# Optimization experiments

Measured on AMD Instinct MI355X. Metric: run time of the kernel, lower is better.

Reference implementation:

```python
import jax, jax.numpy as jnp
import numpy as np

H = 150  # hidden size
I = 1    # input size


def setup_inputs() -> dict:
    key = jax.random.key(0)
    ks = jax.random.split(key, 7)
    B, T = 512, 1024
    s_ih = 1.0 / np.sqrt(H)
    x = jax.random.normal(ks[0], (B, T, I), dtype=jnp.float32)
    # PyTorch LSTM params, gate order (i, f, g, o) stacked along first dim
    W_ih = jax.random.uniform(ks[1], (4 * H, I), jnp.float32, -s_ih, s_ih)
    W_hh = jax.random.uniform(ks[2], (4 * H, H), jnp.float32, -s_ih, s_ih)
    b_ih = jax.random.uniform(ks[3], (4 * H,), jnp.float32, -s_ih, s_ih)
    b_hh = jax.random.uniform(ks[4], (4 * H,), jnp.float32, -s_ih, s_ih)
    # final Linear(150 -> 1)
    W_out = jax.random.uniform(ks[5], (1, H), jnp.float32, -s_ih, s_ih)
    b_out = jax.random.uniform(ks[6], (1,), jnp.float32, -s_ih, s_ih)
    return {"x": x, "W_ih": W_ih, "W_hh": W_hh, "b_ih": b_ih,
            "b_hh": b_hh, "W_out": W_out, "b_out": b_out}


def _lstm_scan(x, W_ih, W_hh, b_ih, b_hh):
    B, T, _ = x.shape
    # precompute input contribution for all timesteps: [T, B, 4H]
    xg = jnp.einsum('bti,gi->tbg', x, W_ih) + (b_ih + b_hh)
    h0 = jnp.zeros((B, H), x.dtype)
    c0 = jnp.zeros((B, H), x.dtype)

    def step(carry, xg_t):
        h, c = carry
        gates = xg_t + h @ W_hh.T  # [B, 4H]
        i, f, g, o = jnp.split(gates, 4, axis=-1)
        i = jax.nn.sigmoid(i)
        f = jax.nn.sigmoid(f)
        g = jnp.tanh(g)
        o = jax.nn.sigmoid(o)
        c = f * c + i * g
        h = o * jnp.tanh(c)
        return (h, c), h

    _, hs = jax.lax.scan(step, (h0, c0), xg)  # hs: [T, B, H]
    return jnp.transpose(hs, (1, 0, 2))       # [B, T, H]


def reference(x, W_ih, W_hh, b_ih, b_hh, W_out, b_out):
    h = _lstm_scan(x, W_ih, W_hh, b_ih, b_hh)          # [B, T, H]
    return jax.nn.sigmoid(h @ W_out.T + b_out)         # [B, T, 1]
```

## Files before the change

### kernel.cpp

```cpp
#include <hip/hip_runtime.h>


typedef _Float16 half8 __attribute__((ext_vector_type(8)));
typedef int int32x8 __attribute__((ext_vector_type(8)));
typedef float f32x4 __attribute__((ext_vector_type(4)));

#define LOG2E 1.44269504088896340736f
#define TWOLOG2E 2.88539008177792681472f

__device__ inline unsigned enc_fp8(float v) {
  const float a = fabsf(v);
  const unsigned s = (__float_as_uint(v) >> 24) & 0x80u;
  const unsigned bits = __float_as_uint(a) + 0x80000u;
  const unsigned code_n = (bits >> 20) - (120u << 3);
  const unsigned code_d = (unsigned)(a * 512.0f + 0.5f);
  const unsigned code = (a < 0.015625f) ? code_d : code_n;
  return s | (code & 0x7Fu);
}

__global__
__attribute__((amdgpu_flat_work_group_size(512, 512), amdgpu_waves_per_eu(2, 2)))
void lstm_kernel(
    const float* __restrict__ x,
    const float* __restrict__ W_ih,
    const float* __restrict__ W_hh,
    const float* __restrict__ b_ih,
    const float* __restrict__ b_hh,
    const float* __restrict__ W_out,
    const float* __restrict__ b_out,
    float* __restrict__ out)
{
  const int tid  = threadIdx.x;
  const int wid  = tid >> 6;
  const int lane = tid & 63;
  const int q    = lane >> 4;
  const int b    = lane & 15;
  const int br   = b & 1;
  const int bid  = blockIdx.x;

  __shared__ __align__(16) _Float16 hbuf[2][2][168];
  __shared__ __align__(64) unsigned char h8[2][2][128];
  __shared__ _Float16 xlds[2][1032];

  for (int i = tid; i < 2*2*168; i += 512)
    (&hbuf[0][0][0])[i] = (_Float16)0.0f;
  if (tid < 128) ((unsigned*)&h8[0][0][0])[tid] = 0u;
  {
    const float4* x4 = (const float4*)(x + (size_t)bid * 2 * 1024);
    const int row = tid >> 8, c4 = tid & 255;
    float4 v = x4[row*256 + c4];
    xlds[row][c4*4+0] = (_Float16)v.x;
    xlds[row][c4*4+1] = (_Float16)v.y;
    xlds[row][c4*4+2] = (_Float16)v.z;
    xlds[row][c4*4+3] = (_Float16)v.w;
  }
  __syncthreads();
  if (tid < 4) hbuf[tid>>1][tid&1][150] = (_Float16)1.0f;
  if (tid < 2) hbuf[0][tid][151] = xlds[tid][0];
  __syncthreads();

  const int NT = (wid < 6) ? 5 : 4;
  const float bo = b_out[0];

  int32x8 wf8[5];
  half8 wf16[5];
#pragma unroll
  for (int j = 0; j < 5; ++j) {
#pragma unroll
    for (int d = 0; d < 8; ++d) wf8[j][d] = 0;
    wf16[j] = (half8)(_Float16)0.0f;
    if (j < NT) {
      const int vrow = (wid + 8*j)*16 + b;
      const int cell = vrow >> 2, gate = vrow & 3;
      const float alpha = (gate == 2) ? TWOLOG2E : -LOG2E;
#pragma unroll
      for (int d = 0; d < 8; ++d) {
        unsigned dw = 0;
#pragma unroll
        for (int c = 0; c < 4; ++c) {
          const int k = q*32 + 4*d + c;
          float w = 0.0f;
          if (vrow == 600)      w = -LOG2E * W_out[k];
          else if (cell < 150)  w = alpha * W_hh[(gate*150 + cell)*150 + k];
          dw |= enc_fp8(w) << (8*c);
        }
        wf8[j][d] = (int)dw;
      }
      half8 v;
#pragma unroll
      for (int jj = 0; jj < 8; ++jj) {
        const int k = 128 + q*8 + jj;
        float w = 0.0f;
        if (vrow == 600) {
          if (k < 150)       w = -LOG2E * W_out[k];
          else if (k == 150) w = -LOG2E * bo;
        } else if (cell < 150) {
          const int orow = gate*150 + cell;
          if (k < 150)       w = alpha * W_hh[orow*150 + k];
          else if (k == 150) w = alpha * (b_ih[orow] + b_hh[orow]);
          else if (k == 151) w = alpha * W_ih[orow];
        }
        v[jj] = (_Float16)w;
      }
      wf16[j] = v;
    }
  }

  float cst = 0.f;
  const int  e     = b >> 1;
  const int  cellm = 4*(wid + 8*e) + q;
  const bool wen   = (e < NT) && (cellm < 150);
  const bool w8    = wen && (cellm < 128);
  const bool w16   = wen && (cellm >= 128);
  const int  wc8   = (cellm < 128) ? cellm : 0;
  const int  wc16  = (cellm >= 128 && cellm < 150) ? cellm : 152;
  const bool is_x  = (wid == 7) && (q == 0) && (b < 2);
  const bool is_out= (wid == 5) && (q == 2) && (b < 2);
  float* outp = out + ((size_t)bid*2 + br) * 1024;

  const unsigned char* p8r0 = &h8[0][br][q*32];
  const unsigned char* p8r1 = &h8[1][br][q*32];
  const _Float16* p16r0 = &hbuf[0][br][128 + q*8];
  const _Float16* p16r1 = &hbuf[1][br][128 + q*8];
  unsigned char* w8p0 = &h8[0][br][wc8];
  unsigned char* w8p1 = &h8[1][br][wc8];
  _Float16* w16p0 = &hbuf[0][br][wc16];
  _Float16* w16p1 = &hbuf[1][br][wc16];
  _Float16* xw0 = &hbuf[0][br][151];
  _Float16* xw1 = &hbuf[1][br][151];
  const f32x4 ZERO = {0.f, 0.f, 0.f, 0.f};

  for (int t = 0; t <= 1024; ++t) {
    _Float16 xv = (_Float16)0.0f;
    if (is_x && t < 1023) xv = xlds[b][t+1];

    const int32x8 bf8 = *(const int32x8*)((t & 1) ? p8r1 : p8r0);
    const half8  bf16 = *(const half8*)((t & 1) ? p16r1 : p16r0);

    f32x4 acc[5];
    __builtin_amdgcn_s_setprio(1);
#pragma unroll
    for (int j = 0; j < 4; ++j) {
      acc[j] = __builtin_amdgcn_mfma_scale_f32_16x16x128_f8f6f4(
                   wf8[j], bf8, ZERO, 0, 0, 0, 0x7F7F7F7F, 0, 0x7F7F7F7F);
      acc[j] = __builtin_amdgcn_mfma_f32_16x16x32_f16(wf16[j], bf16, acc[j], 0,0,0);
    }
    if (wid < 6) {
      acc[4] = __builtin_amdgcn_mfma_scale_f32_16x16x128_f8f6f4(
                   wf8[4], bf8, ZERO, 0, 0, 0, 0x7F7F7F7F, 0, 0x7F7F7F7F);
      acc[4] = __builtin_amdgcn_mfma_f32_16x16x32_f16(wf16[4], bf16, acc[4], 0,0,0);
    } else {
      acc[4] = ZERO;
    }
    __builtin_amdgcn_s_setprio(0);

    if (is_out && t >= 1)
      outp[t-1] = __builtin_amdgcn_rcpf(1.0f + __builtin_amdgcn_exp2f(acc[4][0]));
    if (t == 1024) break;

    f32x4 g;
#pragma unroll
    for (int r = 0; r < 4; ++r) {
      const float t01 = (b & 2) ? acc[1][r] : acc[0][r];
      const float t23 = (b & 2) ? acc[3][r] : acc[2][r];
      const float t03 = (b & 4) ? t23 : t01;
      g[r] = (b & 8) ? acc[4][r] : t03;
    }
    const float ei = __builtin_amdgcn_exp2f(g[0]);
    const float ef = __builtin_amdgcn_exp2f(g[1]);
    const float eg = __builtin_amdgcn_exp2f(g[2]);
    const float eo = __builtin_amdgcn_exp2f(g[3]);
    const float A   = 1.0f + ei;
    const float F   = 1.0f + ef;
    const float G1  = eg + 1.0f;
    const float Gm  = eg - 1.0f;
    const float AG  = A * G1;
    const float num = fmaf(cst, AG, Gm * F);
    const float cn  = num * __builtin_amdgcn_rcpf(F * AG);
    cst = cn;
    const float ec = __builtin_amdgcn_exp2f(TWOLOG2E * cn);
    const float hv = (ec - 1.0f) *
                     __builtin_amdgcn_rcpf((1.0f + eo) * (ec + 1.0f));
    if (w8) {
      unsigned char* w = (t & 1) ? w8p0 : w8p1;
      *w = (unsigned char)enc_fp8(hv);
    }
    if (w16) {
      _Float16* w = (t & 1) ? w16p0 : w16p1;
      *w = (_Float16)hv;
    }
    if (is_x && t < 1023) {
      _Float16* xw = (t & 1) ? xw0 : xw1;
      *xw = xv;
    }
    __syncthreads();
  }
}

extern "C" void kernel_launch(void* const* d_in, const int* in_sizes, int n_in,
                              void* d_out, int out_size, void* d_ws, size_t ws_size,
                              hipStream_t stream) {
  const float* x     = (const float*)d_in[0];
  const float* W_ih  = (const float*)d_in[1];
  const float* W_hh  = (const float*)d_in[2];
  const float* b_ih  = (const float*)d_in[3];
  const float* b_hh  = (const float*)d_in[4];
  const float* W_out = (const float*)d_in[5];
  const float* b_out = (const float*)d_in[6];
  lstm_kernel<<<dim3(256), dim3(512), 0, stream>>>(
      x, W_ih, W_hh, b_ih, b_hh, W_out, b_out, (float*)d_out);
}
```

Measured before the change: 616.6 us.

## Unroll LSTM time loop by four, batch output stores, use hardware fp8 convert

Unrolls the recurrent time loop four steps at a time, so buffer parity and step indices become compile-time constants and the per-step branching goes away. The sigmoid outputs are kept in registers and written as one float4 every four steps, with the final step handled after the loop. The per-step software fp8 encoding of h is replaced with the hardware cvt_pk_fp8_f32 builtin when it is available. The goal is fewer ALU and scalar instructions on the serial critical path, at the cost of larger code, higher register pressure, and possible rounding or saturation differences between the hardware converter and the manual encoder.

```diff
diff --git a/kernel.cpp b/kernel.cpp
--- a/kernel.cpp
+++ b/kernel.cpp
@@ -8,7 +8,7 @@
 #define LOG2E 1.44269504088896340736f
 #define TWOLOG2E 2.88539008177792681472f
 
-__device__ inline unsigned enc_fp8(float v) {
+__device__ inline unsigned enc_fp8_manual(float v) {
   const float a = fabsf(v);
   const unsigned s = (__float_as_uint(v) >> 24) & 0x80u;
   const unsigned bits = __float_as_uint(a) + 0x80000u;
@@ -16,6 +16,14 @@
   const unsigned code_d = (unsigned)(a * 512.0f + 0.5f);
   const unsigned code = (a < 0.015625f) ? code_d : code_n;
   return s | (code & 0x7Fu);
+}
+
+__device__ inline unsigned char enc8(float v) {
+#if __has_builtin(__builtin_amdgcn_cvt_pk_fp8_f32)
+  return (unsigned char)(__builtin_amdgcn_cvt_pk_fp8_f32(v, v, 0, false) & 0xFF);
+#else
+  return (unsigned char)enc_fp8_manual(v);
+#endif
 }
 
 __global__
@@ -82,7 +90,7 @@
           float w = 0.0f;
           if (vrow == 600)      w = -LOG2E * W_out[k];
           else if (cell < 150)  w = alpha * W_hh[(gate*150 + cell)*150 + k];
-          dw |= enc_fp8(w) << (8*c);
+          dw |= enc_fp8_manual(w) << (8*c);
         }
         wf8[j][d] = (int)dw;
       }
@@ -128,72 +136,86 @@
   _Float16* w16p1 = &hbuf[1][br][wc16];
   _Float16* xw0 = &hbuf[0][br][151];
   _Float16* xw1 = &hbuf[1][br][151];
+  const _Float16* xq = &xlds[b & 1][0];
   const f32x4 ZERO = {0.f, 0.f, 0.f, 0.f};
 
-  for (int t = 0; t <= 1024; ++t) {
-    _Float16 xv = (_Float16)0.0f;
-    if (is_x && t < 1023) xv = xlds[b][t+1];
-
-    const int32x8 bf8 = *(const int32x8*)((t & 1) ? p8r1 : p8r0);
-    const half8  bf16 = *(const half8*)((t & 1) ? p16r1 : p16r0);
-
-    f32x4 acc[5];
-    __builtin_amdgcn_s_setprio(1);
-#pragma unroll
-    for (int j = 0; j < 4; ++j) {
-      acc[j] = __builtin_amdgcn_mfma_scale_f32_16x16x128_f8f6f4(
-                   wf8[j], bf8, ZERO, 0, 0, 0, 0x7F7F7F7F, 0, 0x7F7F7F7F);
-      acc[j] = __builtin_amdgcn_mfma_f32_16x16x32_f16(wf16[j], bf16, acc[j], 0,0,0);
+  float o0 = 0.f, o1 = 0.f, o2 = 0.f, o3 = 0.f;
+
+#define STEP_BODY(U, PAR, OREG, OGATE)                                        \
+  {                                                                           \
+    _Float16 xv = (_Float16)0.0f;                                             \
+    if (is_x && (U) < 1023) xv = xq[(U) + 1];                                 \
+    const int32x8 bf8 = *(const int32x8*)((PAR) ? p8r1 : p8r0);               \
+    const half8 bf16  = *(const half8*)((PAR) ? p16r1 : p16r0);               \
+    f32x4 acc[5];                                                             \
+    __builtin_amdgcn_s_setprio(1);                                            \
+    _Pragma("unroll")                                                         \
+    for (int j = 0; j < 4; ++j) {                                             \
+      acc[j] = __builtin_amdgcn_mfma_scale_f32_16x16x128_f8f6f4(              \
+                   wf8[j], bf8, ZERO, 0, 0, 0, 0x7F7F7F7F, 0, 0x7F7F7F7F);    \
+      acc[j] = __builtin_amdgcn_mfma_f32_16x16x32_f16(wf16[j], bf16,          \
+                                                      acc[j], 0, 0, 0);       \
+    }                                                                         \
+    if (wid < 6) {                                                            \
+      acc[4] = __builtin_amdgcn_mfma_scale_f32_16x16x128_f8f6f4(              \
+                   wf8[4], bf8, ZERO, 0, 0, 0, 0x7F7F7F7F, 0, 0x7F7F7F7F);    \
+      acc[4] = __builtin_amdgcn_mfma_f32_16x16x32_f16(wf16[4], bf16,          \
+                                                      acc[4], 0, 0, 0);       \
+    } else {                                                                  \
+      acc[4] = ZERO;                                                          \
+    }                                                                         \
+    __builtin_amdgcn_s_setprio(0);                                            \
+    if (is_out && (OGATE))                                                    \
+      OREG = __builtin_amdgcn_rcpf(1.0f + __builtin_amdgcn_exp2f(acc[4][0])); \
+                         \
+    f32x4 g;                                                                  \
+    _Pragma("unroll")                                                         \
+    for (int r = 0; r < 4; ++r) {                                             \
+      const float t01 = (b & 2) ? acc[1][r] : acc[0][r];                      \
+      const float t23 = (b & 2) ? acc[3][r] : acc[2][r];                      \
+      const float t03 = (b & 4) ? t23 : t01;                                  \
+      g[r] = (b & 8) ? acc[4][r] : t03;                                       \
+    }                                                                         \
+    const float ei = __builtin_amdgcn_exp2f(g[0]);                            \
+    const float ef = __builtin_amdgcn_exp2f(g[1]);                            \
+    const float eg = __builtin_amdgcn_exp2f(g[2]);                            \
+    const float eo = __builtin_amdgcn_exp2f(g[3]);                            \
+    const float A   = 1.0f + ei;                                              \
+    const float F   = 1.0f + ef;                                              \
+    const float G1  = eg + 1.0f;                                              \
+    const float Gm  = eg - 1.0f;                                              \
+    const float AG  = A * G1;                                                 \
+    const float num = fmaf(cst, AG, Gm * F);                                  \
+    const float cn  = num * __builtin_amdgcn_rcpf(F * AG);                    \
+    cst = cn;                                                                 \
+    const float ec = __builtin_amdgcn_exp2f(TWOLOG2E * cn);                   \
+    const float hv = (ec - 1.0f) *                                            \
+                     __builtin_amdgcn_rcpf((1.0f + eo) * (ec + 1.0f));        \
+    if (w8)  *((PAR) ? w8p0 : w8p1) = enc8(hv);                               \
+    if (w16) *((PAR) ? w16p0 : w16p1) = (_Float16)hv;                         \
+    if (is_x && (U) < 1023) *((PAR) ? xw0 : xw1) = xv;                        \
+    __syncthreads();                                                          \
+  }
+
+  for (int t = 0; t < 1024; t += 4) {
+    STEP_BODY(t + 0, 0, o3, t > 0)
+    if (is_out && t >= 4)
+      *(float4*)(outp + t - 4) = (float4){o0, o1, o2, o3};
+    STEP_BODY(t + 1, 1, o0, 1)
+    STEP_BODY(t + 2, 0, o1, 1)
+    STEP_BODY(t + 3, 1, o2, 1)
+  }
+
+  if (wid == 5) {
+    const int32x8 bf8 = *(const int32x8*)p8r0;
+    const half8 bf16  = *(const half8*)p16r0;
+    f32x4 a = __builtin_amdgcn_mfma_scale_f32_16x16x128_f8f6f4(
+                  wf8[4], bf8, ZERO, 0, 0, 0, 0x7F7F7F7F, 0, 0x7F7F7F7F);
+    a = __builtin_amdgcn_mfma_f32_16x16x32_f16(wf16[4], bf16, a, 0, 0, 0);
+    if (is_out) {
+      o3 = __builtin_amdgcn_rcpf(1.0f + __builtin_amdgcn_exp2f(a[0]));
+      *(float4*)(outp + 1020) = (float4){o0, o1, o2, o3};
     }
-    if (wid < 6) {
-      acc[4] = __builtin_amdgcn_mfma_scale_f32_16x16x128_f8f6f4(
-                   wf8[4], bf8, ZERO, 0, 0, 0, 0x7F7F7F7F, 0, 0x7F7F7F7F);
-      acc[4] = __builtin_amdgcn_mfma_f32_16x16x32_f16(wf16[4], bf16, acc[4], 0,0,0);
-    } else {
-      acc[4] = ZERO;
-    }
-    __builtin_amdgcn_s_setprio(0);
-
-    if (is_out && t >= 1)
-      outp[t-1] = __builtin_amdgcn_rcpf(1.0f + __builtin_amdgcn_exp2f(acc[4][0]));
-    if (t == 1024) break;
-
-    f32x4 g;
-#pragma unroll
-    for (int r = 0; r < 4; ++r) {
-      const float t01 = (b & 2) ? acc[1][r] : acc[0][r];
-      const float t23 = (b & 2) ? acc[3][r] : acc[2][r];
-      const float t03 = (b & 4) ? t23 : t01;
-      g[r] = (b & 8) ? acc[4][r] : t03;
-    }
-    const float ei = __builtin_amdgcn_exp2f(g[0]);
-    const float ef = __builtin_amdgcn_exp2f(g[1]);
-    const float eg = __builtin_amdgcn_exp2f(g[2]);
-    const float eo = __builtin_amdgcn_exp2f(g[3]);
-    const float A   = 1.0f + ei;
-    const float F   = 1.0f + ef;
-    const float G1  = eg + 1.0f;
-    const float Gm  = eg - 1.0f;
-    const float AG  = A * G1;
-    const float num = fmaf(cst, AG, Gm * F);
-    const float cn  = num * __builtin_amdgcn_rcpf(F * AG);
-    cst = cn;
-    const float ec = __builtin_amdgcn_exp2f(TWOLOG2E * cn);
-    const float hv = (ec - 1.0f) *
-                     __builtin_amdgcn_rcpf((1.0f + eo) * (ec + 1.0f));
-    if (w8) {
-      unsigned char* w = (t & 1) ? w8p0 : w8p1;
-      *w = (unsigned char)enc_fp8(hv);
-    }
-    if (w16) {
-      _Float16* w = (t & 1) ? w16p0 : w16p1;
-      *w = (_Float16)hv;
-    }
-    if (is_x && t < 1023) {
-      _Float16* xw = (t & 1) ? xw0 : xw1;
-      *xw = xv;
-    }
-    __syncthreads();
   }
 }
 
```

Measured after the change: 539.3 us. 12.5% less time.
